# Kernel optimization log

Measured on AMD Instinct MI355X. Metric: run time of the kernel, lower is better.

The kernel has to match this reference:

```python
import jax, jax.numpy as jnp
import numpy as np

NEG_SLOPE = 0.01  # nn.LeakyReLU default


def leaky_relu(x):
    return jnp.where(x >= 0, x, NEG_SLOPE * x)


def gcn_conv(x, W, b, src, dst, n_nodes):
    """PyG GCNConv: add self loops, symmetric D^-1/2 (A+I) D^-1/2 norm, then x @ W + b."""
    h = x @ W  # [N, D]
    # degree with self-loops (edge weight 1 each, +1 for the self loop)
    deg = jnp.zeros((n_nodes,), dtype=x.dtype).at[dst].add(1.0) + 1.0
    dinv = jax.lax.rsqrt(deg)  # deg >= 1 thanks to self loops
    norm = dinv[src] * dinv[dst]  # [E]
    msg = h[src] * norm[:, None]  # gather + scale, [E, D]
    agg = jnp.zeros_like(h).at[dst].add(msg)  # scatter-add over targets
    agg = agg + h * (dinv * dinv)[:, None]  # self-loop contribution
    return agg + b


def setup_inputs() -> dict:
    key = jax.random.key(0)
    ks = jax.random.split(key, 12)
    N, E = 100000, 640000
    ND, D, C = 239, 128, 2
    x = jax.random.normal(ks[0], (N, ND), dtype=jnp.float32)
    edge_index = jax.random.randint(ks[1], (2, E), 0, N, dtype=jnp.int64)
    edge_type = jax.random.randint(ks[2], (E,), 0, 4, dtype=jnp.int64)
    s = 0.05
    W_in = jax.random.normal(ks[3], (ND, D), dtype=jnp.float32) * s
    b_in = jax.random.normal(ks[4], (D,), dtype=jnp.float32) * s
    W_g = jax.random.normal(ks[5], (D, D), dtype=jnp.float32) * s
    b_g = jax.random.normal(ks[6], (D,), dtype=jnp.float32) * s
    W_o1 = jax.random.normal(ks[7], (D, D), dtype=jnp.float32) * s
    b_o1 = jax.random.normal(ks[8], (D,), dtype=jnp.float32) * s
    W_o2 = jax.random.normal(ks[9], (D, C), dtype=jnp.float32) * s
    b_o2 = jax.random.normal(ks[10], (C,), dtype=jnp.float32) * s
    return {"x": x, "edge_index": edge_index, "edge_type": edge_type,
            "W_in": W_in, "b_in": b_in, "W_g": W_g, "b_g": b_g,
            "W_o1": W_o1, "b_o1": b_o1, "W_o2": W_o2, "b_o2": b_o2}


def reference(x, edge_index, edge_type, W_in, b_in, W_g, b_g, W_o1, b_o1, W_o2, b_o2):
    n_nodes = x.shape[0]
    src, dst = edge_index[0], edge_index[1]
    h = leaky_relu(x @ W_in + b_in)
    h = gcn_conv(h, W_g, b_g, src, dst, n_nodes)
    # dropout is identity in eval mode (training=False)
    h = gcn_conv(h, W_g, b_g, src, dst, n_nodes)  # same shared GCNConv instance
    h = leaky_relu(h @ W_o1 + b_o1)
    return h @ W_o2 + b_o2
```

## Files before the change

kernel.cpp:

```cpp
#include <hip/hip_runtime.h>
#include <hip/hip_bf16.h>


typedef __attribute__((ext_vector_type(8))) __bf16 bf16x8;
typedef __attribute__((ext_vector_type(4))) float f32x4;

__global__ __launch_bounds__(256) void wtr_k(const float* __restrict__ W, ushort* __restrict__ Wt,
                                             int K, int Kp) {
  int idx = blockIdx.x * 256 + threadIdx.x;
  if (idx >= 128 * Kp) return;
  int n = idx / Kp, k = idx % Kp;
  float v = (k < K) ? W[(size_t)k * 128 + n] : 0.f;
  __hip_bfloat16 h = __float2bfloat16(v);
  Wt[idx] = *(ushort*)&h;
}


__global__ __launch_bounds__(256) void zero_k(int* __restrict__ p, int n) {
  int i = blockIdx.x * 256 + threadIdx.x;
  if (i < n) p[i] = 0;
}

__global__ __launch_bounds__(256) void hist_k(const int* __restrict__ dst, int* __restrict__ cnt, int E) {
  int e = blockIdx.x * 256 + threadIdx.x;
  if (e < E) atomicAdd(&cnt[dst[e]], 1);
}

__global__ __launch_bounds__(256) void scan1_k(const int* __restrict__ cnt, int* __restrict__ rp,
                                               int* __restrict__ bsum, int N) {
  __shared__ int sd[256];
  int t = threadIdx.x;
  int base = blockIdx.x * 1024 + t * 4;
  int v0 = (base + 0 < N) ? cnt[base + 0] : 0;
  int v1 = (base + 1 < N) ? cnt[base + 1] : 0;
  int v2 = (base + 2 < N) ? cnt[base + 2] : 0;
  int v3 = (base + 3 < N) ? cnt[base + 3] : 0;
  int ts = v0 + v1 + v2 + v3;
  sd[t] = ts;
  __syncthreads();
  for (int off = 1; off < 256; off <<= 1) {
    int y = (t >= off) ? sd[t - off] : 0;
    __syncthreads();
    sd[t] += y;
    __syncthreads();
  }
  int x = sd[t] - ts;
  if (t == 255) bsum[blockIdx.x] = sd[255];
  if (base + 0 < N) rp[base + 0] = x; x += v0;
  if (base + 1 < N) rp[base + 1] = x; x += v1;
  if (base + 2 < N) rp[base + 2] = x; x += v2;
  if (base + 3 < N) rp[base + 3] = x;
}

__global__ __launch_bounds__(256) void scan2_k(int* __restrict__ bsum, int NB) {
  __shared__ int sd[256];
  int t = threadIdx.x;
  int base = t * 4;
  int v0 = (base + 0 < NB) ? bsum[base + 0] : 0;
  int v1 = (base + 1 < NB) ? bsum[base + 1] : 0;
  int v2 = (base + 2 < NB) ? bsum[base + 2] : 0;
  int v3 = (base + 3 < NB) ? bsum[base + 3] : 0;
  int ts = v0 + v1 + v2 + v3;
  sd[t] = ts;
  __syncthreads();
  for (int off = 1; off < 256; off <<= 1) {
    int y = (t >= off) ? sd[t - off] : 0;
    __syncthreads();
    sd[t] += y;
    __syncthreads();
  }
  int x = sd[t] - ts;
  if (base + 0 < NB) bsum[base + 0] = x; x += v0;
  if (base + 1 < NB) bsum[base + 1] = x; x += v1;
  if (base + 2 < NB) bsum[base + 2] = x; x += v2;
  if (base + 3 < NB) bsum[base + 3] = x;
}

__global__ __launch_bounds__(256) void scan3_k(int* __restrict__ rp, int* __restrict__ pos,
                                               const int* __restrict__ bsum,
                                               float* __restrict__ dinv, int N, int E) {
  int i = blockIdx.x * 256 + threadIdx.x;
  if (i < N) {
    int c = pos[i];
    int v = rp[i] + bsum[i >> 10];
    dinv[i] = rsqrtf((float)c + 1.0f);
    rp[i] = v;
    pos[i] = v;
  }
  if (i == 0) rp[N] = E;
}

__global__ __launch_bounds__(256) void fill_k(const int* __restrict__ src, const int* __restrict__ dst,
                                              const float* __restrict__ dinv,
                                              int* __restrict__ pos, int2* __restrict__ ew, int E) {
  int e = blockIdx.x * 256 + threadIdx.x;
  if (e < E) {
    int d = dst[e];
    int s = src[e];
    int idx = atomicAdd(&pos[d], 1);
    ew[idx] = make_int2(s, __float_as_int(dinv[s] * dinv[d]));
  }
}


__global__ __launch_bounds__(512, 4) void gemm1_k(const float* __restrict__ x,
                                                  const ushort* __restrict__ Wt,
                                                  const float* __restrict__ bias,
                                                  ushort* __restrict__ C, int N, int Ka,
                                                  unsigned long long M ) {
  __shared__ ushort Al[128 * 248];
  __shared__ ushort Wl[128 * 72];
  const int tid = threadIdx.x;
  const int wave = tid >> 6;
  const int lane = tid & 63;
  const int l16 = lane & 15;
  const int quad = lane >> 4;
  const int m0 = blockIdx.x * 128;

  if (tid < 128) {
    Al[tid * 248 + 239] = 0;
    *(uint4*)&Al[tid * 248 + 240] = make_uint4(0, 0, 0, 0);
  }

  {
    int rows = N - m0;
    if (rows > 128) rows = 128;
    const int region = rows * Ka;
    const float* __restrict__ xb = x + (size_t)m0 * Ka;
    const int nv4 = region >> 2;
    for (int i = tid; i < nv4; i += 512) {
      float4 v = ((const float4*)xb)[i];
      int f0 = i * 4;
      float vf[4] = {v.x, v.y, v.z, v.w};
#pragma unroll
      for (int j = 0; j < 4; ++j) {
        int idx = f0 + j;
        uint r = (uint)(((unsigned long long)(uint)idx * M) >> 40);
        uint c = (uint)idx - r * (uint)Ka;
        __hip_bfloat16 h = __float2bfloat16(vf[j]);
        Al[r * 248 + c] = *(ushort*)&h;
      }
    }
    for (int i = (nv4 << 2) + tid; i < region; i += 512) {
      uint r = (uint)(((unsigned long long)(uint)i * M) >> 40);
      uint c = (uint)i - r * (uint)Ka;
      __hip_bfloat16 h = __float2bfloat16(xb[i]);
      Al[r * 248 + c] = *(ushort*)&h;
    }
  }

  f32x4 acc[8] = {};
  const int wn = tid >> 2;
  const int wseg = tid & 3;
#pragma unroll
  for (int kc = 0; kc < 4; ++kc) {
    __syncthreads();
    *(uint4*)&Wl[wn * 72 + wseg * 16] =
        *(const uint4*)(Wt + (size_t)wn * 256 + kc * 64 + wseg * 16);
    *(uint4*)&Wl[wn * 72 + wseg * 16 + 8] =
        *(const uint4*)(Wt + (size_t)wn * 256 + kc * 64 + wseg * 16 + 8);
    __syncthreads();
#pragma unroll
    for (int s = 0; s < 2; ++s) {
      const int koff = kc * 64 + s * 32 + quad * 8;
      bf16x8 a = {};
      if (koff < 248) a = *(const bf16x8*)&Al[(wave * 16 + l16) * 248 + koff];
      const int wof = s * 32 + quad * 8;
#pragma unroll
      for (int c = 0; c < 8; ++c) {
        bf16x8 b = *(const bf16x8*)&Wl[(c * 16 + l16) * 72 + wof];
        acc[c] = __builtin_amdgcn_mfma_f32_16x16x32_bf16(a, b, acc[c], 0, 0, 0);
      }
    }
  }

  float bv[8];
#pragma unroll
  for (int c = 0; c < 8; ++c) bv[c] = bias[c * 16 + l16];
#pragma unroll
  for (int reg = 0; reg < 4; ++reg) {
    int row = m0 + wave * 16 + quad * 4 + reg;
    if (row < N) {
#pragma unroll
      for (int c = 0; c < 8; ++c) {
        float v = acc[c][reg] + bv[c];
        v = v >= 0.f ? v : 0.01f * v;
        __hip_bfloat16 h = __float2bfloat16(v);
        C[(size_t)row * 128 + c * 16 + l16] = *(ushort*)&h;
      }
    }
  }
}


template <int MODE>
__global__ __launch_bounds__(512, 4) void mgemm_k(const ushort* __restrict__ A,
                                                  const ushort* __restrict__ Wt,
                                                  const float* __restrict__ bias,
                                                  const float* __restrict__ W2,
                                                  const float* __restrict__ b2,
                                                  void* __restrict__ C, int N) {
  __shared__ uint4 Al[128 * 16];
  __shared__ uint4 Wl[128 * 16];
  const int tid = threadIdx.x;
  const int wave = tid >> 6;
  const int lane = tid & 63;
  const int l16 = lane & 15;
  const int quad = lane >> 4;
  const int m0 = blockIdx.x * 128;

  f32x4 acc[8] = {};
  const int r_s = tid >> 4;
  const int j8 = tid & 15;
#pragma unroll
  for (int it = 0; it < 4; ++it) {
    int m = it * 32 + r_s;
    Al[m * 16 + (j8 ^ (m & 15))] = *(const uint4*)(A + (size_t)(m0 + m) * 128 + j8 * 8);
  }
#pragma unroll
  for (int it = 0; it < 4; ++it) {
    int n = it * 32 + r_s;
    Wl[n * 16 + (j8 ^ (n & 15))] = *(const uint4*)(Wt + (size_t)n * 128 + j8 * 8);
  }
  __syncthreads();
#pragma unroll
  for (int s = 0; s < 4; ++s) {
    const int j = s * 4 + quad;
    const int arow = wave * 16 + l16;
    bf16x8 a = *(const bf16x8*)&Al[arow * 16 + (j ^ (arow & 15))];
#pragma unroll
    for (int c = 0; c < 8; ++c) {
      const int brow = c * 16 + l16;
      bf16x8 b = *(const bf16x8*)&Wl[brow * 16 + (j ^ (brow & 15))];
      acc[c] = __builtin_amdgcn_mfma_f32_16x16x32_bf16(a, b, acc[c], 0, 0, 0);
    }
  }

  float bv[8];
#pragma unroll
  for (int c = 0; c < 8; ++c) bv[c] = bias[c * 16 + l16];

  if constexpr (MODE == 3) {
    float w20[8], w21[8];
#pragma unroll
    for (int c = 0; c < 8; ++c) {
      int colj = c * 16 + l16;
      w20[c] = W2[colj * 2 + 0];
      w21[c] = W2[colj * 2 + 1];
    }
    float bb0 = b2[0], bb1 = b2[1];
#pragma unroll
    for (int reg = 0; reg < 4; ++reg) {
      float o0 = 0.f, o1 = 0.f;
#pragma unroll
      for (int c = 0; c < 8; ++c) {
        float v = acc[c][reg] + bv[c];
        v = v >= 0.f ? v : 0.01f * v;
        o0 = fmaf(v, w20[c], o0);
        o1 = fmaf(v, w21[c], o1);
      }
      o0 += __shfl_xor(o0, 1); o0 += __shfl_xor(o0, 2);
      o0 += __shfl_xor(o0, 4); o0 += __shfl_xor(o0, 8);
      o1 += __shfl_xor(o1, 1); o1 += __shfl_xor(o1, 2);
      o1 += __shfl_xor(o1, 4); o1 += __shfl_xor(o1, 8);
      int row = m0 + wave * 16 + quad * 4 + reg;
      if (l16 == 0 && row < N)
        *(float2*)((float*)C + (size_t)row * 2) = make_float2(o0 + bb0, o1 + bb1);
    }
    return;
  }

#pragma unroll
  for (int reg = 0; reg < 4; ++reg) {
    int row = m0 + wave * 16 + quad * 4 + reg;
    if (row < N) {
#pragma unroll
      for (int c = 0; c < 8; ++c) {
        float v = acc[c][reg] + bv[c];
        __hip_bfloat16 h = __float2bfloat16(v);
        ((ushort*)C)[(size_t)row * 128 + c * 16 + l16] = *(ushort*)&h;
      }
    }
  }
}


__global__ __launch_bounds__(256) void agg_k(const ushort* __restrict__ T,
                                             const float* __restrict__ dinv,
                                             const int* __restrict__ rp,
                                             const int2* __restrict__ ew,
                                             ushort* __restrict__ O, int N) {
  int l = threadIdx.x & 15;
  int node = blockIdx.x * 16 + (threadIdx.x >> 4);
  if (node >= N) return;
  float di = dinv[node];
  float dsq = di * di;
  const uint4* T4 = (const uint4*)T;
  float a[8];
  {
    uint4 sv = T4[(size_t)node * 16 + l];
    uint u[4] = {sv.x, sv.y, sv.z, sv.w};
#pragma unroll
    for (int p = 0; p < 4; ++p) {
      a[2 * p + 0] = __uint_as_float(u[p] << 16) * dsq;
      a[2 * p + 1] = __uint_as_float(u[p] & 0xFFFF0000u) * dsq;
    }
  }
  int e1 = rp[node + 1];
  for (int e = rp[node]; e < e1; ++e) {
    int2 pw = ew[e];
    float w = __int_as_float(pw.y);
    uint4 v = T4[(size_t)pw.x * 16 + l];
    uint u[4] = {v.x, v.y, v.z, v.w};
#pragma unroll
    for (int p = 0; p < 4; ++p) {
      a[2 * p + 0] = fmaf(__uint_as_float(u[p] << 16), w, a[2 * p + 0]);
      a[2 * p + 1] = fmaf(__uint_as_float(u[p] & 0xFFFF0000u), w, a[2 * p + 1]);
    }
  }
  union { uint4 v; ushort s[8]; } uo;
#pragma unroll
  for (int j = 0; j < 8; ++j) {
    __hip_bfloat16 h = __float2bfloat16(a[j]);
    uo.s[j] = *(ushort*)&h;
  }
  ((uint4*)O)[(size_t)node * 16 + l] = uo.v;
}


extern "C" void kernel_launch(void* const* d_in, const int* in_sizes, int n_in,
                              void* d_out, int out_size, void* d_ws, size_t ws_size,
                              hipStream_t stream) {
  const float* x = (const float*)d_in[0];
  const int* ei = (const int*)d_in[1];
  const float* W_in = (const float*)d_in[3];
  const float* b_in = (const float*)d_in[4];
  const float* W_g  = (const float*)d_in[5];
  const float* b_g  = (const float*)d_in[6];
  const float* W_o1 = (const float*)d_in[7];
  const float* b_o1 = (const float*)d_in[8];
  const float* W_o2 = (const float*)d_in[9];
  const float* b_o2 = (const float*)d_in[10];

  const int D = in_sizes[4];
  const int ND = in_sizes[3] / D;
  const int N = in_sizes[0] / ND;
  const int E = in_sizes[2];
  const int* src = ei;
  const int* dst = ei + E;

  const int N_pad = ((N + 127) / 128) * 128;
  const size_t np = (size_t)N_pad;
  const int KP1 = 256;
  const unsigned long long MAGIC = ((1ULL << 40) + (unsigned)ND - 1) / (unsigned)ND;

  ushort* hA = (ushort*)d_ws;
  ushort* hB = hA + np * 128;
  ushort* Wt_in = hB + np * 128;
  ushort* Wt_g  = Wt_in + 128 * 256;
  ushort* Wt_o1 = Wt_g + 128 * 128;
  float* dinv = (float*)(Wt_o1 + 128 * 128);
  int* cnt  = (int*)(dinv + N);
  int* rp   = cnt + N;
  int* bsum = rp + (N + 1);
  int2* ew  = (int2*)(((size_t)(bsum + 1024) + 7) & ~(size_t)7);

  const int NB = (N + 1023) / 1024;

  wtr_k<<<(128 * KP1 + 255) / 256, 256, 0, stream>>>(W_in, Wt_in, ND, KP1);
  wtr_k<<<(128 * 128 + 255) / 256, 256, 0, stream>>>(W_g, Wt_g, 128, 128);
  wtr_k<<<(128 * 128 + 255) / 256, 256, 0, stream>>>(W_o1, Wt_o1, 128, 128);

  zero_k<<<(N + 255) / 256, 256, 0, stream>>>(cnt, N);
  hist_k<<<(E + 255) / 256, 256, 0, stream>>>(dst, cnt, E);
  scan1_k<<<NB, 256, 0, stream>>>(cnt, rp, bsum, N);
  scan2_k<<<1, 256, 0, stream>>>(bsum, NB);
  scan3_k<<<(N + 255) / 256, 256, 0, stream>>>(rp, cnt , bsum, dinv, N, E);
  fill_k<<<(E + 255) / 256, 256, 0, stream>>>(src, dst, dinv, cnt, ew, E);

  const int gblocks = N_pad / 128;
  const int ablocks = (N + 15) / 16;
  gemm1_k<<<gblocks, 512, 0, stream>>>(x, Wt_in, b_in, hA, N, ND, MAGIC);
  agg_k<<<ablocks, 256, 0, stream>>>(hA, dinv, rp, ew, hB, N);
  mgemm_k<1><<<gblocks, 512, 0, stream>>>(hB, Wt_g, b_g, nullptr, nullptr, hA, N);
  agg_k<<<ablocks, 256, 0, stream>>>(hA, dinv, rp, ew, hB, N);
  mgemm_k<1><<<gblocks, 512, 0, stream>>>(hB, Wt_g, b_g, nullptr, nullptr, hA, N);
  mgemm_k<3><<<gblocks, 512, 0, stream>>>(hA, Wt_o1, b_o1, W_o2, b_o2, d_out, N);
}
```

Baseline: 365.7 us.

## Stage x via global_load_lds in first GEMM, unroll aggregation, merge weight transposes

The first GEMM now copies raw fp32 x rows straight into LDS with global_load_lds and converts to bf16 when reading MFMA operands. The tile drops to 64 rows, so two waves share each row block and split the 128 output columns. This replaces the per-element magic-division scatter into a bf16 LDS tile. The aggregation loop is unrolled by four (with two- and one-edge tails) so several neighbour gathers are in flight at once, and the three weight-transpose launches become one. The costs are repeated fp32-to-bf16 conversion in the inner loop, possible LDS bank conflicts from the unpadded Ka stride, and higher register use in the aggregation kernel.

```diff
diff --git a/kernel.cpp b/kernel.cpp
--- a/kernel.cpp
+++ b/kernel.cpp
@@ -5,14 +5,32 @@
 typedef __attribute__((ext_vector_type(8))) __bf16 bf16x8;
 typedef __attribute__((ext_vector_type(4))) float f32x4;
 
-__global__ __launch_bounds__(256) void wtr_k(const float* __restrict__ W, ushort* __restrict__ Wt,
-                                             int K, int Kp) {
+typedef __attribute__((address_space(1))) const void gvoid_t;
+typedef __attribute__((address_space(3))) void svoid_t;
+
+__global__ __launch_bounds__(256) void wtr_all_k(const float* __restrict__ W_in,
+                                                 const float* __restrict__ W_g,
+                                                 const float* __restrict__ W_o1,
+                                                 ushort* __restrict__ Wt_in,
+                                                 ushort* __restrict__ Wt_g,
+                                                 ushort* __restrict__ Wt_o1, int ND) {
   int idx = blockIdx.x * 256 + threadIdx.x;
-  if (idx >= 128 * Kp) return;
-  int n = idx / Kp, k = idx % Kp;
-  float v = (k < K) ? W[(size_t)k * 128 + n] : 0.f;
-  __hip_bfloat16 h = __float2bfloat16(v);
-  Wt[idx] = *(ushort*)&h;
+  if (idx < 128 * 256) {
+    int n = idx >> 8, k = idx & 255;
+    float v = (k < ND) ? W_in[(size_t)k * 128 + n] : 0.f;
+    __hip_bfloat16 h = __float2bfloat16(v);
+    Wt_in[idx] = *(ushort*)&h;
+  } else if (idx < 128 * 256 + 128 * 128) {
+    int j = idx - 128 * 256;
+    int n = j >> 7, k = j & 127;
+    __hip_bfloat16 h = __float2bfloat16(W_g[(size_t)k * 128 + n]);
+    Wt_g[j] = *(ushort*)&h;
+  } else if (idx < 128 * 256 + 2 * 128 * 128) {
+    int j = idx - 128 * 256 - 128 * 128;
+    int n = j >> 7, k = j & 127;
+    __hip_bfloat16 h = __float2bfloat16(W_o1[(size_t)k * 128 + n]);
+    Wt_o1[j] = *(ushort*)&h;
+  }
 }
 
 
@@ -106,50 +124,35 @@
 __global__ __launch_bounds__(512, 4) void gemm1_k(const float* __restrict__ x,
                                                   const ushort* __restrict__ Wt,
                                                   const float* __restrict__ bias,
-                                                  ushort* __restrict__ C, int N, int Ka,
-                                                  unsigned long long M ) {
-  __shared__ ushort Al[128 * 248];
+                                                  ushort* __restrict__ C, int N, int Ka) {
+  __shared__ float Af[64 * 239 + 8];
   __shared__ ushort Wl[128 * 72];
   const int tid = threadIdx.x;
   const int wave = tid >> 6;
   const int lane = tid & 63;
   const int l16 = lane & 15;
   const int quad = lane >> 4;
-  const int m0 = blockIdx.x * 128;
-
-  if (tid < 128) {
-    Al[tid * 248 + 239] = 0;
-    *(uint4*)&Al[tid * 248 + 240] = make_uint4(0, 0, 0, 0);
-  }
+  const int m0 = blockIdx.x * 64;
 
   {
     int rows = N - m0;
-    if (rows > 128) rows = 128;
-    const int region = rows * Ka;
-    const float* __restrict__ xb = x + (size_t)m0 * Ka;
-    const int nv4 = region >> 2;
-    for (int i = tid; i < nv4; i += 512) {
-      float4 v = ((const float4*)xb)[i];
-      int f0 = i * 4;
-      float vf[4] = {v.x, v.y, v.z, v.w};
-#pragma unroll
-      for (int j = 0; j < 4; ++j) {
-        int idx = f0 + j;
-        uint r = (uint)(((unsigned long long)(uint)idx * M) >> 40);
-        uint c = (uint)idx - r * (uint)Ka;
-        __hip_bfloat16 h = __float2bfloat16(vf[j]);
-        Al[r * 248 + c] = *(ushort*)&h;
-      }
-    }
-    for (int i = (nv4 << 2) + tid; i < region; i += 512) {
-      uint r = (uint)(((unsigned long long)(uint)i * M) >> 40);
-      uint c = (uint)i - r * (uint)Ka;
-      __hip_bfloat16 h = __float2bfloat16(xb[i]);
-      Al[r * 248 + c] = *(ushort*)&h;
-    }
-  }
-
-  f32x4 acc[8] = {};
+    if (rows > 64) rows = 64;
+    const int nwords = rows * Ka;
+    const float* __restrict__ gsrc = x + (size_t)m0 * Ka;
+    const int nchunks = nwords >> 8;
+    for (int ch = wave; ch < nchunks; ch += 8) {
+      __builtin_amdgcn_global_load_lds(
+          (gvoid_t*)(gsrc + ch * 256 + lane * 4),
+          (svoid_t*)(&Af[ch * 256]), 16, 0, 0);
+    }
+    for (int i = (nchunks << 8) + tid; i < nwords; i += 512) {
+      Af[i] = gsrc[i];
+    }
+  }
+
+  f32x4 acc[4] = {};
+  const int wr = wave >> 1;
+  const int wc = wave & 1;
   const int wn = tid >> 2;
   const int wseg = tid & 3;
 #pragma unroll
@@ -164,29 +167,44 @@
     for (int s = 0; s < 2; ++s) {
       const int koff = kc * 64 + s * 32 + quad * 8;
       bf16x8 a = {};
-      if (koff < 248) a = *(const bf16x8*)&Al[(wave * 16 + l16) * 248 + koff];
+      const float* ap = &Af[(wr * 16 + l16) * Ka + koff];
+      if (koff + 8 <= Ka) {
+#pragma unroll
+        for (int j = 0; j < 8; ++j) {
+          __hip_bfloat16 h = __float2bfloat16(ap[j]);
+          a[j] = *(__bf16*)&h;
+        }
+      } else if (koff < Ka) {
+#pragma unroll
+        for (int j = 0; j < 8; ++j) {
+          if (koff + j < Ka) {
+            __hip_bfloat16 h = __float2bfloat16(ap[j]);
+            a[j] = *(__bf16*)&h;
+          }
+        }
+      }
       const int wof = s * 32 + quad * 8;
 #pragma unroll
-      for (int c = 0; c < 8; ++c) {
-        bf16x8 b = *(const bf16x8*)&Wl[(c * 16 + l16) * 72 + wof];
+      for (int c = 0; c < 4; ++c) {
+        bf16x8 b = *(const bf16x8*)&Wl[(wc * 64 + c * 16 + l16) * 72 + wof];
         acc[c] = __builtin_amdgcn_mfma_f32_16x16x32_bf16(a, b, acc[c], 0, 0, 0);
       }
     }
   }
 
-  float bv[8];
-#pragma unroll
-  for (int c = 0; c < 8; ++c) bv[c] = bias[c * 16 + l16];
+  float bv[4];
+#pragma unroll
+  for (int c = 0; c < 4; ++c) bv[c] = bias[wc * 64 + c * 16 + l16];
 #pragma unroll
   for (int reg = 0; reg < 4; ++reg) {
-    int row = m0 + wave * 16 + quad * 4 + reg;
+    int row = m0 + wr * 16 + quad * 4 + reg;
     if (row < N) {
 #pragma unroll
-      for (int c = 0; c < 8; ++c) {
+      for (int c = 0; c < 4; ++c) {
         float v = acc[c][reg] + bv[c];
         v = v >= 0.f ? v : 0.01f * v;
         __hip_bfloat16 h = __float2bfloat16(v);
-        C[(size_t)row * 128 + c * 16 + l16] = *(ushort*)&h;
+        C[(size_t)row * 128 + wc * 64 + c * 16 + l16] = *(ushort*)&h;
       }
     }
   }
@@ -306,8 +324,49 @@
       a[2 * p + 1] = __uint_as_float(u[p] & 0xFFFF0000u) * dsq;
     }
   }
-  int e1 = rp[node + 1];
-  for (int e = rp[node]; e < e1; ++e) {
+  int e = rp[node];
+  const int e1 = rp[node + 1];
+  for (; e + 4 <= e1; e += 4) {
+    int2 p0 = ew[e + 0], p1 = ew[e + 1], p2 = ew[e + 2], p3 = ew[e + 3];
+    uint4 v0 = T4[(size_t)p0.x * 16 + l];
+    uint4 v1 = T4[(size_t)p1.x * 16 + l];
+    uint4 v2 = T4[(size_t)p2.x * 16 + l];
+    uint4 v3 = T4[(size_t)p3.x * 16 + l];
+    float w0 = __int_as_float(p0.y), w1 = __int_as_float(p1.y);
+    float w2 = __int_as_float(p2.y), w3 = __int_as_float(p3.y);
+    uint u0[4] = {v0.x, v0.y, v0.z, v0.w};
+    uint u1[4] = {v1.x, v1.y, v1.z, v1.w};
+    uint u2[4] = {v2.x, v2.y, v2.z, v2.w};
+    uint u3[4] = {v3.x, v3.y, v3.z, v3.w};
+#pragma unroll
+    for (int p = 0; p < 4; ++p) {
+      a[2 * p + 0] = fmaf(__uint_as_float(u0[p] << 16), w0, a[2 * p + 0]);
+      a[2 * p + 1] = fmaf(__uint_as_float(u0[p] & 0xFFFF0000u), w0, a[2 * p + 1]);
+      a[2 * p + 0] = fmaf(__uint_as_float(u1[p] << 16), w1, a[2 * p + 0]);
+      a[2 * p + 1] = fmaf(__uint_as_float(u1[p] & 0xFFFF0000u), w1, a[2 * p + 1]);
+      a[2 * p + 0] = fmaf(__uint_as_float(u2[p] << 16), w2, a[2 * p + 0]);
+      a[2 * p + 1] = fmaf(__uint_as_float(u2[p] & 0xFFFF0000u), w2, a[2 * p + 1]);
+      a[2 * p + 0] = fmaf(__uint_as_float(u3[p] << 16), w3, a[2 * p + 0]);
+      a[2 * p + 1] = fmaf(__uint_as_float(u3[p] & 0xFFFF0000u), w3, a[2 * p + 1]);
+    }
+  }
+  if (e + 2 <= e1) {
+    int2 p0 = ew[e + 0], p1 = ew[e + 1];
+    uint4 v0 = T4[(size_t)p0.x * 16 + l];
+    uint4 v1 = T4[(size_t)p1.x * 16 + l];
+    float w0 = __int_as_float(p0.y), w1 = __int_as_float(p1.y);
+    uint u0[4] = {v0.x, v0.y, v0.z, v0.w};
+    uint u1[4] = {v1.x, v1.y, v1.z, v1.w};
+#pragma unroll
+    for (int p = 0; p < 4; ++p) {
+      a[2 * p + 0] = fmaf(__uint_as_float(u0[p] << 16), w0, a[2 * p + 0]);
+      a[2 * p + 1] = fmaf(__uint_as_float(u0[p] & 0xFFFF0000u), w0, a[2 * p + 1]);
+      a[2 * p + 0] = fmaf(__uint_as_float(u1[p] << 16), w1, a[2 * p + 0]);
+      a[2 * p + 1] = fmaf(__uint_as_float(u1[p] & 0xFFFF0000u), w1, a[2 * p + 1]);
+    }
+    e += 2;
+  }
+  if (e < e1) {
     int2 pw = ew[e];
     float w = __int_as_float(pw.y);
     uint4 v = T4[(size_t)pw.x * 16 + l];
@@ -352,7 +411,6 @@
   const int N_pad = ((N + 127) / 128) * 128;
   const size_t np = (size_t)N_pad;
   const int KP1 = 256;
-  const unsigned long long MAGIC = ((1ULL << 40) + (unsigned)ND - 1) / (unsigned)ND;
 
   ushort* hA = (ushort*)d_ws;
   ushort* hB = hA + np * 128;
@@ -367,9 +425,8 @@
 
   const int NB = (N + 1023) / 1024;
 
-  wtr_k<<<(128 * KP1 + 255) / 256, 256, 0, stream>>>(W_in, Wt_in, ND, KP1);
-  wtr_k<<<(128 * 128 + 255) / 256, 256, 0, stream>>>(W_g, Wt_g, 128, 128);
-  wtr_k<<<(128 * 128 + 255) / 256, 256, 0, stream>>>(W_o1, Wt_o1, 128, 128);
+  wtr_all_k<<<(128 * KP1 + 2 * 128 * 128 + 255) / 256, 256, 0, stream>>>(
+      W_in, W_g, W_o1, Wt_in, Wt_g, Wt_o1, ND);
 
   zero_k<<<(N + 255) / 256, 256, 0, stream>>>(cnt, N);
   hist_k<<<(E + 255) / 256, 256, 0, stream>>>(dst, cnt, E);
@@ -378,9 +435,10 @@
   scan3_k<<<(N + 255) / 256, 256, 0, stream>>>(rp, cnt , bsum, dinv, N, E);
   fill_k<<<(E + 255) / 256, 256, 0, stream>>>(src, dst, dinv, cnt, ew, E);
 
+  const int g1blocks = (N + 63) / 64;
   const int gblocks = N_pad / 128;
   const int ablocks = (N + 15) / 16;
-  gemm1_k<<<gblocks, 512, 0, stream>>>(x, Wt_in, b_in, hA, N, ND, MAGIC);
+  gemm1_k<<<g1blocks, 512, 0, stream>>>(x, Wt_in, b_in, hA, N, ND);
   agg_k<<<ablocks, 256, 0, stream>>>(hA, dinv, rp, ew, hB, N);
   mgemm_k<1><<<gblocks, 512, 0, stream>>>(hB, Wt_g, b_g, nullptr, nullptr, hA, N);
   agg_k<<<ablocks, 256, 0, stream>>>(hA, dinv, rp, ew, hB, N);
```

After: 347.4 us. 5.0% less time.
